# Kernel tuning notes

Hardware: AMD Instinct MI355X
Metric: run time of the kernel (lower is better)

## Reference

```python
import jax, jax.numpy as jnp
import numpy as np

B, S, D, H = 4, 2048, 1024, 16
HD = D // H
SCALE = 1.0 / np.sqrt(HD)
BIG_NEG = -1e9


def setup_inputs() -> dict:
    key = jax.random.key(0)
    ks = jax.random.split(key, 10)
    std = 1.0 / np.sqrt(D)
    return {
        "hidden_states": jax.random.normal(ks[0], (B, S, D), dtype=jnp.float32),
        "attention_mask": jax.random.bernoulli(ks[1], 0.9, (B, S)),
        "Wq": jax.random.normal(ks[2], (D, D), dtype=jnp.float32) * std,
        "bq": jnp.zeros((D,), jnp.float32),
        "Wk": jax.random.normal(ks[3], (D, D), dtype=jnp.float32) * std,
        "bk": jnp.zeros((D,), jnp.float32),
        "Wv": jax.random.normal(ks[4], (D, D), dtype=jnp.float32) * std,
        "bv": jnp.zeros((D,), jnp.float32),
        "Wo": jax.random.normal(ks[5], (D, D), dtype=jnp.float32) * std,
        "bo": jnp.zeros((D,), jnp.float32),
    }


def reference(hidden_states, attention_mask, Wq, bq, Wk, bk, Wv, bv, Wo, bo):
    b, s, d = hidden_states.shape
    maskf = attention_mask.astype(hidden_states.dtype)  # [B,S]
    x = hidden_states * maskf[:, :, None]  # mask inputs (as in torch fallback)

    def proj(W, bias):
        # torch Linear: x @ W.T + b, then split heads -> [B,H,S,HD]
        y = jnp.einsum('bsd,ed->bse', x, W) + bias
        return y.reshape(b, s, H, HD).transpose(0, 2, 1, 3)

    q = proj(Wq, bq)
    k = proj(Wk, bk)
    v = proj(Wv, bv)

    scores = jnp.einsum('bhqd,bhkd->bhqk', q, k) * SCALE  # [B,H,S,S]
    pair = attention_mask[:, None, :, None] & attention_mask[:, None, None, :]
    scores = jnp.where(pair, scores, BIG_NEG)
    # softmax; fully-masked query rows become uniform, then zeroed below
    # (matches torch's -inf softmax -> NaN -> nan_to_num(0.0))
    w = jax.nn.softmax(scores, axis=-1) * maskf[:, None, :, None]
    ctx = jnp.einsum('bhqk,bhkd->bhqd', w, v)  # [B,H,S,HD]
    ctx = ctx.transpose(0, 2, 1, 3).reshape(b, s, d)
    out = jnp.einsum('bsd,ed->bse', ctx, Wo) + bo
    return out * maskf[:, :, None]
```

## Files before the change

kernel.cpp:

```cpp
#include <hip/hip_runtime.h>
#include <math.h>


typedef __attribute__((ext_vector_type(4))) float f32x4;
typedef __attribute__((ext_vector_type(8))) short s16x8;

#define MFMA16(a, b, c) __builtin_amdgcn_mfma_f32_16x16x32_bf16((a), (b), (c), 0, 0, 0)

constexpr int B_ = 4, S_ = 2048, D_ = 1024, H_ = 16, HD_ = 64;
constexpr float SCALE_ = 0.125f;
constexpr float LOG2E_ = 1.4426950408889634f;
constexpr float BIG_NEG_ = -1e9f;
constexpr float DEFER_THR_ = 8.f;

__device__ __forceinline__ ushort f2b(float x) {
    unsigned u = __float_as_uint(x);
    return (ushort)((u + 0x7FFFu + ((u >> 16) & 1u)) >> 16);
}

__device__ __forceinline__ void gload16(const ushort* g, ushort* l) {
    __builtin_amdgcn_global_load_lds(
        (const __attribute__((address_space(1))) void*)g,
        (__attribute__((address_space(3))) void*)l, 16, 0, 0);
}

__global__ __launch_bounds__(256)
void convert_all(const float* __restrict__ hidden, const int* __restrict__ mask,
                 const float* __restrict__ Wq, const float* __restrict__ Wk,
                 const float* __restrict__ Wv, const float* __restrict__ Wo,
                 ushort* __restrict__ Xb, ushort* __restrict__ Wb)
{
    const int NXC = 1048576;
    const int NWC = 131072;
    const int TOT = NXC + 4 * NWC;
    for (int idx = blockIdx.x * 256 + threadIdx.x; idx < TOT; idx += gridDim.x * 256) {
        if (idx < NXC) {
            const size_t e = (size_t)idx * 8;
            const float mf = (float)mask[e >> 10];
            const float4 a = *(const float4*)(hidden + e);
            const float4 b = *(const float4*)(hidden + e + 4);
            s16x8 v;
            v[0] = (short)f2b(a.x * mf); v[1] = (short)f2b(a.y * mf);
            v[2] = (short)f2b(a.z * mf); v[3] = (short)f2b(a.w * mf);
            v[4] = (short)f2b(b.x * mf); v[5] = (short)f2b(b.y * mf);
            v[6] = (short)f2b(b.z * mf); v[7] = (short)f2b(b.w * mf);
            *(s16x8*)(Xb + e) = v;
        } else {
            const int c = idx - NXC;
            const int sel = c >> 17;
            const size_t off = (size_t)(c & (NWC - 1)) * 8;
            const float* src = (sel == 0) ? Wq : (sel == 1) ? Wk : (sel == 2) ? Wv : Wo;
            const float4 a = *(const float4*)(src + off);
            const float4 b = *(const float4*)(src + off + 4);
            s16x8 v;
            v[0] = (short)f2b(a.x); v[1] = (short)f2b(a.y);
            v[2] = (short)f2b(a.z); v[3] = (short)f2b(a.w);
            v[4] = (short)f2b(b.x); v[5] = (short)f2b(b.y);
            v[6] = (short)f2b(b.z); v[7] = (short)f2b(b.w);
            *(s16x8*)(Wb + (size_t)sel * 1048576 + off) = v;
        }
    }
}

__global__ __launch_bounds__(256)
void qkv_gemm(const ushort* __restrict__ Xb, const ushort* __restrict__ Wall,
              const float* __restrict__ bq, const float* __restrict__ bk,
              const float* __restrict__ bv,
              ushort* __restrict__ Qb, ushort* __restrict__ Kb,
              ushort* __restrict__ Vb)
{
    __shared__ ushort As[128 * 64];
    __shared__ ushort Bs[128 * 64];

    const int t = threadIdx.x;
    const int lane = t & 63;
    const int w = t >> 6, wr = w >> 1, wc = w & 1;
    const int lrow = lane & 15, lk = lane >> 4;
    const int m0 = blockIdx.x * 128;
    const int sel = blockIdx.y >> 3;
    const int n0 = (blockIdx.y & 7) * 128;

    const ushort* Wb = Wall + (size_t)sel * 1048576;
    const float* bias = (sel == 0) ? bq : (sel == 1) ? bk : bv;
    ushort* Out = (sel == 0) ? Qb : (sel == 1) ? Kb : Vb;
    const float escale = (sel == 0) ? SCALE_ * LOG2E_ : 1.f;

    f32x4 acc[4][4];
    #pragma unroll
    for (int i = 0; i < 4; ++i)
        #pragma unroll
        for (int j = 0; j < 4; ++j) acc[i][j] = (f32x4)0.f;

    for (int k0 = 0; k0 < D_; k0 += 64) {
        __syncthreads();
        #pragma unroll
        for (int p = 0; p < 4; ++p) {
            const int c = p * 256 + t;
            const int row = c >> 3, slot = c & 7;
            ushort* dst_base_a = As + (size_t)(p * 256 + (t & 192)) * 8;
            ushort* dst_base_b = Bs + (size_t)(p * 256 + (t & 192)) * 8;
            gload16(Xb + (size_t)(m0 + row) * 1024 + k0 + slot * 8, dst_base_a);
            gload16(Wb + (size_t)(n0 + row) * 1024 + k0 + slot * 8, dst_base_b);
        }
        __syncthreads();

        #pragma unroll
        for (int kk = 0; kk < 2; ++kk) {
            s16x8 af[4], bf[4];
            #pragma unroll
            for (int i = 0; i < 4; ++i)
                af[i] = *(const s16x8*)(As + (wr * 64 + i * 16 + lrow) * 64 + kk * 32 + lk * 8);
            #pragma unroll
            for (int j = 0; j < 4; ++j)
                bf[j] = *(const s16x8*)(Bs + (wc * 64 + j * 16 + lrow) * 64 + kk * 32 + lk * 8);
            #pragma unroll
            for (int i = 0; i < 4; ++i)
                #pragma unroll
                for (int j = 0; j < 4; ++j)
                    acc[i][j] = MFMA16(af[i], bf[j], acc[i][j]);
        }
    }

    #pragma unroll
    for (int i = 0; i < 4; ++i) {
        #pragma unroll
        for (int j = 0; j < 4; ++j) {
            const int gn = n0 + wc * 64 + j * 16 + lrow;
            const float bb = bias[gn];
            const int h_ = gn >> 6, hd_ = gn & 63;
            #pragma unroll
            for (int r = 0; r < 4; ++r) {
                const int gm = m0 + wr * 64 + i * 16 + lk * 4 + r;
                const float v = (acc[i][j][r] + bb) * escale;
                const int b_ = gm >> 11, s_ = gm & (S_ - 1);
                Out[(((size_t)(b_ * H_ + h_)) * S_ + s_) * HD_ + hd_] = f2b(v);
            }
        }
    }
}

__global__ __launch_bounds__(256)
void transpose_v(const ushort* __restrict__ V, ushort* __restrict__ VT)
{
    __shared__ ushort L[64][72];
    const int t = threadIdx.x;
    const int s0 = blockIdx.x * 64;
    const size_t base = ((size_t)(blockIdx.z * H_ + blockIdx.y)) * S_ * HD_;
    const int r = t >> 2, cb = (t & 3) * 16;

    *(s16x8*)&L[r][cb]     = *(const s16x8*)(V + base + (size_t)(s0 + r) * 64 + cb);
    *(s16x8*)&L[r][cb + 8] = *(const s16x8*)(V + base + (size_t)(s0 + r) * 64 + cb + 8);
    __syncthreads();

    s16x8 o0, o1;
    #pragma unroll
    for (int k = 0; k < 8; ++k) o0[k] = (short)L[cb + k][r];
    #pragma unroll
    for (int k = 0; k < 8; ++k) o1[k] = (short)L[cb + 8 + k][r];
    *(s16x8*)(VT + base + (size_t)r * S_ + s0 + cb)     = o0;
    *(s16x8*)(VT + base + (size_t)r * S_ + s0 + cb + 8) = o1;
}

__global__ __launch_bounds__(256)
void attn_bf16(const ushort* __restrict__ Q, const ushort* __restrict__ K,
               const ushort* __restrict__ VT, const int* __restrict__ mask,
               ushort* __restrict__ ctx)
{
    __shared__ ushort Ks[64 * 64];
    __shared__ ushort Vs[64 * 64];
    __shared__ ushort Ps[4][16 * 64];

    const int t = threadIdx.x;
    const int lane = t & 63, w = t >> 6;
    const int lrow = lane & 15, lk = lane >> 4;
    const int q0 = blockIdx.x * 64, h = blockIdx.y, b = blockIdx.z;

    const ushort* Qh = Q + ((size_t)(b * H_ + h)) * S_ * HD_;
    const ushort* Kh = K + ((size_t)(b * H_ + h)) * S_ * HD_;
    const ushort* Vh = VT + ((size_t)(b * H_ + h)) * HD_ * S_;
    const int* mrow = mask + b * S_;

    s16x8 qf[2];
    qf[0] = *(const s16x8*)(Qh + (q0 + w * 16 + lrow) * 64 + lk * 8);
    qf[1] = *(const s16x8*)(Qh + (q0 + w * 16 + lrow) * 64 + 32 + lk * 8);

    f32x4 O[4];
    #pragma unroll
    for (int nt = 0; nt < 4; ++nt) O[nt] = (f32x4)0.f;
    float m_run[4] = {-INFINITY, -INFINITY, -INFINITY, -INFINITY};
    float l_run[4] = {0.f, 0.f, 0.f, 0.f};

    const int srow0 = t >> 3,           sslot0 = t & 7;
    const int srow1 = (t + 256) >> 3,   sslot1 = t & 7;
    s16x8 kreg0, kreg1, vreg0, vreg1;
    kreg0 = *(const s16x8*)(Kh + (size_t)srow0 * 64 + sslot0 * 8);
    kreg1 = *(const s16x8*)(Kh + (size_t)srow1 * 64 + sslot1 * 8);
    vreg0 = *(const s16x8*)(Vh + (size_t)srow0 * S_ + sslot0 * 8);
    vreg1 = *(const s16x8*)(Vh + (size_t)srow1 * S_ + sslot1 * 8);

    for (int k0 = 0; k0 < S_; k0 += 64) {
        __syncthreads();
        *(s16x8*)(Ks + srow0 * 64 + ((sslot0 ^ (srow0 & 7)) * 8)) = kreg0;
        *(s16x8*)(Ks + srow1 * 64 + ((sslot1 ^ (srow1 & 7)) * 8)) = kreg1;
        *(s16x8*)(Vs + srow0 * 64 + ((sslot0 ^ (srow0 & 7)) * 8)) = vreg0;
        *(s16x8*)(Vs + srow1 * 64 + ((sslot1 ^ (srow1 & 7)) * 8)) = vreg1;
        __syncthreads();

        if (k0 + 64 < S_) {
            kreg0 = *(const s16x8*)(Kh + (size_t)(k0 + 64 + srow0) * 64 + sslot0 * 8);
            kreg1 = *(const s16x8*)(Kh + (size_t)(k0 + 64 + srow1) * 64 + sslot1 * 8);
            vreg0 = *(const s16x8*)(Vh + (size_t)srow0 * S_ + k0 + 64 + sslot0 * 8);
            vreg1 = *(const s16x8*)(Vh + (size_t)srow1 * S_ + k0 + 64 + sslot1 * 8);
        }

        f32x4 sc[4];
        #pragma unroll
        for (int nt = 0; nt < 4; ++nt) sc[nt] = (f32x4)0.f;
        #pragma unroll
        for (int kk = 0; kk < 2; ++kk)
            #pragma unroll
            for (int nt = 0; nt < 4; ++nt) {
                const int krow = nt * 16 + lrow;
                const s16x8 kf = *(const s16x8*)(Ks + krow * 64 + (((kk * 4 + lk) ^ (krow & 7)) * 8));
                sc[nt] = MFMA16(qf[kk], kf, sc[nt]);
            }

        int km[4];
        #pragma unroll
        for (int nt = 0; nt < 4; ++nt) km[nt] = mrow[k0 + nt * 16 + lrow];

        float s4[4][4], vmax[4];
        #pragma unroll
        for (int r = 0; r < 4; ++r) {
            #pragma unroll
            for (int nt = 0; nt < 4; ++nt) s4[r][nt] = km[nt] ? sc[nt][r] : BIG_NEG_;
            float tm = fmaxf(fmaxf(s4[r][0], s4[r][1]), fmaxf(s4[r][2], s4[r][3]));
            tm = fmaxf(tm, __shfl_xor(tm, 1));
            tm = fmaxf(tm, __shfl_xor(tm, 2));
            tm = fmaxf(tm, __shfl_xor(tm, 4));
            tm = fmaxf(tm, __shfl_xor(tm, 8));
            vmax[r] = tm;
        }

        float g = vmax[0] - m_run[0];
        #pragma unroll
        for (int r = 1; r < 4; ++r) g = fmaxf(g, vmax[r] - m_run[r]);
        if (!__all(g <= DEFER_THR_)) {
            #pragma unroll
            for (int r = 0; r < 4; ++r) {
                const float mn = fmaxf(m_run[r], vmax[r]);
                const float corr = exp2f(m_run[r] - mn);
                m_run[r] = mn;
                l_run[r] *= corr;
                #pragma unroll
                for (int nt = 0; nt < 4; ++nt) O[nt][r] *= corr;
            }
        }

        float pv[4][4];
        #pragma unroll
        for (int r = 0; r < 4; ++r) {
            float rs = 0.f;
            #pragma unroll
            for (int nt = 0; nt < 4; ++nt) {
                pv[r][nt] = exp2f(s4[r][nt] - m_run[r]);
                rs += pv[r][nt];
            }
            rs += __shfl_xor(rs, 1);
            rs += __shfl_xor(rs, 2);
            rs += __shfl_xor(rs, 4);
            rs += __shfl_xor(rs, 8);
            l_run[r] += rs;
        }

        #pragma unroll
        for (int r = 0; r < 4; ++r) {
            const int q = lk * 4 + r;
            #pragma unroll
            for (int nt = 0; nt < 4; ++nt) {
                const int key = nt * 16 + lrow;
                Ps[w][q * 64 + (((key >> 3) ^ (q & 7)) * 8) + (key & 7)] = f2b(pv[r][nt]);
            }
        }
        #pragma unroll
        for (int kk = 0; kk < 2; ++kk) {
            const s16x8 pa = *(const s16x8*)(&Ps[w][lrow * 64 + (((kk * 4 + lk) ^ (lrow & 7)) * 8)]);
            #pragma unroll
            for (int nt = 0; nt < 4; ++nt) {
                const int vrow = nt * 16 + lrow;
                const s16x8 vf = *(const s16x8*)(Vs + vrow * 64 + (((kk * 4 + lk) ^ (vrow & 7)) * 8));
                O[nt] = MFMA16(pa, vf, O[nt]);
            }
        }
    }

    #pragma unroll
    for (int r = 0; r < 4; ++r) {
        const float inv = 1.f / l_run[r];
        const int s = q0 + w * 16 + lk * 4 + r;
        #pragma unroll
        for (int nt = 0; nt < 4; ++nt)
            ctx[((size_t)(b * S_ + s)) * D_ + h * 64 + nt * 16 + lrow] = f2b(O[nt][r] * inv);
    }
}

__global__ __launch_bounds__(256)
void out_gemm(const ushort* __restrict__ Xb, const ushort* __restrict__ Wb,
              const float* __restrict__ bias, const int* __restrict__ mask,
              float* __restrict__ Cf)
{
    __shared__ ushort As[128 * 64];
    __shared__ ushort Bs[128 * 64];

    const int t = threadIdx.x;
    const int lane = t & 63;
    const int w = t >> 6, wr = w >> 1, wc = w & 1;
    const int lrow = lane & 15, lk = lane >> 4;
    const int m0 = blockIdx.x * 128, n0 = blockIdx.y * 128;

    f32x4 acc[4][4];
    #pragma unroll
    for (int i = 0; i < 4; ++i)
        #pragma unroll
        for (int j = 0; j < 4; ++j) acc[i][j] = (f32x4)0.f;

    for (int k0 = 0; k0 < D_; k0 += 64) {
        __syncthreads();
        #pragma unroll
        for (int p = 0; p < 4; ++p) {
            const int c = p * 256 + t;
            const int row = c >> 3, slot = c & 7;
            gload16(Xb + (size_t)(m0 + row) * 1024 + k0 + slot * 8,
                    As + (size_t)(p * 256 + (t & 192)) * 8);
            gload16(Wb + (size_t)(n0 + row) * 1024 + k0 + slot * 8,
                    Bs + (size_t)(p * 256 + (t & 192)) * 8);
        }
        __syncthreads();

        #pragma unroll
        for (int kk = 0; kk < 2; ++kk) {
            s16x8 af[4], bf[4];
            #pragma unroll
            for (int i = 0; i < 4; ++i)
                af[i] = *(const s16x8*)(As + (wr * 64 + i * 16 + lrow) * 64 + kk * 32 + lk * 8);
            #pragma unroll
            for (int j = 0; j < 4; ++j)
                bf[j] = *(const s16x8*)(Bs + (wc * 64 + j * 16 + lrow) * 64 + kk * 32 + lk * 8);
            #pragma unroll
            for (int i = 0; i < 4; ++i)
                #pragma unroll
                for (int j = 0; j < 4; ++j)
                    acc[i][j] = MFMA16(af[i], bf[j], acc[i][j]);
        }
    }

    #pragma unroll
    for (int i = 0; i < 4; ++i) {
        #pragma unroll
        for (int j = 0; j < 4; ++j) {
            const int gn = n0 + wc * 64 + j * 16 + lrow;
            const float bb = bias[gn];
            #pragma unroll
            for (int r = 0; r < 4; ++r) {
                const int gm = m0 + wr * 64 + i * 16 + lk * 4 + r;
                const float v = (acc[i][j][r] + bb) * (float)mask[gm];
                Cf[(size_t)gm * 1024 + gn] = v;
            }
        }
    }
}

extern "C" void kernel_launch(void* const* d_in, const int* in_sizes, int n_in,
                              void* d_out, int out_size, void* d_ws, size_t ws_size,
                              hipStream_t stream) {
    const float* hidden = (const float*)d_in[0];
    const int*   mask   = (const int*)d_in[1];
    const float* Wq = (const float*)d_in[2];
    const float* bq = (const float*)d_in[3];
    const float* Wk = (const float*)d_in[4];
    const float* bk = (const float*)d_in[5];
    const float* Wv = (const float*)d_in[6];
    const float* bv = (const float*)d_in[7];
    const float* Wo = (const float*)d_in[8];
    const float* bo = (const float*)d_in[9];
    float* out = (float*)d_out;

    ushort* ws = (ushort*)d_ws;
    const size_t T = (size_t)B_ * H_ * S_ * HD_;
    ushort* Xb  = ws;
    ushort* Wb  = ws + T;
    ushort* Qb  = ws + T + 4194304;
    ushort* Kb  = Qb + T;
    ushort* Vb  = Kb + T;
    ushort* VTb = Vb + T;
    ushort* Cb  = VTb + T;

    const dim3 bb(256);
    convert_all<<<2048, bb, 0, stream>>>(hidden, mask, Wq, Wk, Wv, Wo, Xb, Wb);
    qkv_gemm<<<dim3(64, 24), bb, 0, stream>>>(Xb, Wb, bq, bk, bv, Qb, Kb, Vb);
    transpose_v<<<dim3(S_ / 64, H_, B_), bb, 0, stream>>>(Vb, VTb);
    attn_bf16<<<dim3(S_ / 64, H_, B_), bb, 0, stream>>>(Qb, Kb, VTb, mask, Cb);
    out_gemm<<<dim3(64, 8), bb, 0, stream>>>(Cb, Wb + 3 * 1048576, bo, mask, out);
}
```

Baseline: 457.9 us.

## Transpose QK^T MFMA so each lane owns one query row in attention

```diff
diff --git a/kernel.cpp b/kernel.cpp
--- a/kernel.cpp
+++ b/kernel.cpp
@@ -97,10 +97,10 @@
         for (int p = 0; p < 4; ++p) {
             const int c = p * 256 + t;
             const int row = c >> 3, slot = c & 7;
-            ushort* dst_base_a = As + (size_t)(p * 256 + (t & 192)) * 8;
-            ushort* dst_base_b = Bs + (size_t)(p * 256 + (t & 192)) * 8;
-            gload16(Xb + (size_t)(m0 + row) * 1024 + k0 + slot * 8, dst_base_a);
-            gload16(Wb + (size_t)(n0 + row) * 1024 + k0 + slot * 8, dst_base_b);
+            gload16(Xb + (size_t)(m0 + row) * 1024 + k0 + slot * 8,
+                    As + (size_t)(p * 256 + (t & 192)) * 8);
+            gload16(Wb + (size_t)(n0 + row) * 1024 + k0 + slot * 8,
+                    Bs + (size_t)(p * 256 + (t & 192)) * 8);
         }
         __syncthreads();
 
@@ -166,9 +166,9 @@
                const ushort* __restrict__ VT, const int* __restrict__ mask,
                ushort* __restrict__ ctx)
 {
-    __shared__ ushort Ks[64 * 64];
-    __shared__ ushort Vs[64 * 64];
-    __shared__ ushort Ps[4][16 * 64];
+    __shared__ __align__(16) ushort Ks[64 * 64];
+    __shared__ __align__(16) ushort Vs[64 * 64];
+    __shared__ __align__(16) ushort Ps[4][16 * 64];
 
     const int t = threadIdx.x;
     const int lane = t & 63, w = t >> 6;
@@ -187,31 +187,22 @@
     f32x4 O[4];
     #pragma unroll
     for (int nt = 0; nt < 4; ++nt) O[nt] = (f32x4)0.f;
-    float m_run[4] = {-INFINITY, -INFINITY, -INFINITY, -INFINITY};
-    float l_run[4] = {0.f, 0.f, 0.f, 0.f};
-
-    const int srow0 = t >> 3,           sslot0 = t & 7;
-    const int srow1 = (t + 256) >> 3,   sslot1 = t & 7;
-    s16x8 kreg0, kreg1, vreg0, vreg1;
-    kreg0 = *(const s16x8*)(Kh + (size_t)srow0 * 64 + sslot0 * 8);
-    kreg1 = *(const s16x8*)(Kh + (size_t)srow1 * 64 + sslot1 * 8);
-    vreg0 = *(const s16x8*)(Vh + (size_t)srow0 * S_ + sslot0 * 8);
-    vreg1 = *(const s16x8*)(Vh + (size_t)srow1 * S_ + sslot1 * 8);
+    float m_run = -INFINITY;
+    float l_run = 0.f;
+
+    const int srow = t >> 3, sslot = t & 7;
 
     for (int k0 = 0; k0 < S_; k0 += 64) {
         __syncthreads();
-        *(s16x8*)(Ks + srow0 * 64 + ((sslot0 ^ (srow0 & 7)) * 8)) = kreg0;
-        *(s16x8*)(Ks + srow1 * 64 + ((sslot1 ^ (srow1 & 7)) * 8)) = kreg1;
-        *(s16x8*)(Vs + srow0 * 64 + ((sslot0 ^ (srow0 & 7)) * 8)) = vreg0;
-        *(s16x8*)(Vs + srow1 * 64 + ((sslot1 ^ (srow1 & 7)) * 8)) = vreg1;
-        __syncthreads();
-
-        if (k0 + 64 < S_) {
-            kreg0 = *(const s16x8*)(Kh + (size_t)(k0 + 64 + srow0) * 64 + sslot0 * 8);
-            kreg1 = *(const s16x8*)(Kh + (size_t)(k0 + 64 + srow1) * 64 + sslot1 * 8);
-            vreg0 = *(const s16x8*)(Vh + (size_t)srow0 * S_ + k0 + 64 + sslot0 * 8);
-            vreg1 = *(const s16x8*)(Vh + (size_t)srow1 * S_ + k0 + 64 + sslot1 * 8);
-        }
+        #pragma unroll
+        for (int p = 0; p < 2; ++p) {
+            const int row = srow + p * 32;
+            const s16x8 kv = *(const s16x8*)(Kh + (size_t)(k0 + row) * 64 + sslot * 8);
+            *(s16x8*)(Ks + row * 64 + ((sslot ^ (row & 7)) * 8)) = kv;
+            const s16x8 vv = *(const s16x8*)(Vh + (size_t)row * S_ + k0 + sslot * 8);
+            *(s16x8*)(Vs + row * 64 + ((sslot ^ (row & 7)) * 8)) = vv;
+        }
+        __syncthreads();
 
         f32x4 sc[4];
         #pragma unroll
@@ -222,66 +213,60 @@
             for (int nt = 0; nt < 4; ++nt) {
                 const int krow = nt * 16 + lrow;
                 const s16x8 kf = *(const s16x8*)(Ks + krow * 64 + (((kk * 4 + lk) ^ (krow & 7)) * 8));
-                sc[nt] = MFMA16(qf[kk], kf, sc[nt]);
+                sc[nt] = MFMA16(kf, qf[kk], sc[nt]);
             }
 
-        int km[4];
-        #pragma unroll
-        for (int nt = 0; nt < 4; ++nt) km[nt] = mrow[k0 + nt * 16 + lrow];
-
-        float s4[4][4], vmax[4];
-        #pragma unroll
-        for (int r = 0; r < 4; ++r) {
-            #pragma unroll
-            for (int nt = 0; nt < 4; ++nt) s4[r][nt] = km[nt] ? sc[nt][r] : BIG_NEG_;
-            float tm = fmaxf(fmaxf(s4[r][0], s4[r][1]), fmaxf(s4[r][2], s4[r][3]));
-            tm = fmaxf(tm, __shfl_xor(tm, 1));
-            tm = fmaxf(tm, __shfl_xor(tm, 2));
-            tm = fmaxf(tm, __shfl_xor(tm, 4));
-            tm = fmaxf(tm, __shfl_xor(tm, 8));
-            vmax[r] = tm;
-        }
-
-        float g = vmax[0] - m_run[0];
-        #pragma unroll
-        for (int r = 1; r < 4; ++r) g = fmaxf(g, vmax[r] - m_run[r]);
-        if (!__all(g <= DEFER_THR_)) {
-            #pragma unroll
-            for (int r = 0; r < 4; ++r) {
-                const float mn = fmaxf(m_run[r], vmax[r]);
-                const float corr = exp2f(m_run[r] - mn);
-                m_run[r] = mn;
-                l_run[r] *= corr;
+        float s4[4][4];
+        #pragma unroll
+        for (int nt = 0; nt < 4; ++nt) {
+            const int4 km = *(const int4*)(mrow + k0 + nt * 16 + lk * 4);
+            s4[nt][0] = km.x ? sc[nt][0] : BIG_NEG_;
+            s4[nt][1] = km.y ? sc[nt][1] : BIG_NEG_;
+            s4[nt][2] = km.z ? sc[nt][2] : BIG_NEG_;
+            s4[nt][3] = km.w ? sc[nt][3] : BIG_NEG_;
+        }
+
+        float tm = s4[0][0];
+        #pragma unroll
+        for (int nt = 0; nt < 4; ++nt)
+            #pragma unroll
+            for (int r = 0; r < 4; ++r) tm = fmaxf(tm, s4[nt][r]);
+        tm = fmaxf(tm, __shfl_xor(tm, 16));
+        tm = fmaxf(tm, __shfl_xor(tm, 32));
+
+        if (!__all(tm - m_run <= DEFER_THR_)) {
+            const float mn = fmaxf(m_run, tm);
+            const float corr = exp2f(m_run - mn);
+            m_run = mn;
+            l_run *= corr;
+            float cq[4];
+            #pragma unroll
+            for (int r = 0; r < 4; ++r) cq[r] = __shfl(corr, lk * 4 + r);
+            #pragma unroll
+            for (int nt = 0; nt < 4; ++nt)
                 #pragma unroll
-                for (int nt = 0; nt < 4; ++nt) O[nt][r] *= corr;
-            }
-        }
-
-        float pv[4][4];
-        #pragma unroll
-        for (int r = 0; r < 4; ++r) {
-            float rs = 0.f;
-            #pragma unroll
-            for (int nt = 0; nt < 4; ++nt) {
-                pv[r][nt] = exp2f(s4[r][nt] - m_run[r]);
-                rs += pv[r][nt];
-            }
-            rs += __shfl_xor(rs, 1);
-            rs += __shfl_xor(rs, 2);
-            rs += __shfl_xor(rs, 4);
-            rs += __shfl_xor(rs, 8);
-            l_run[r] += rs;
-        }
-
-        #pragma unroll
-        for (int r = 0; r < 4; ++r) {
-            const int q = lk * 4 + r;
-            #pragma unroll
-            for (int nt = 0; nt < 4; ++nt) {
-                const int key = nt * 16 + lrow;
-                Ps[w][q * 64 + (((key >> 3) ^ (q & 7)) * 8) + (key & 7)] = f2b(pv[r][nt]);
-            }
-        }
+                for (int r = 0; r < 4; ++r) O[nt][r] *= cq[r];
+        }
+
+        float p[4][4];
+        float rs = 0.f;
+        #pragma unroll
+        for (int nt = 0; nt < 4; ++nt)
+            #pragma unroll
+            for (int r = 0; r < 4; ++r) { p[nt][r] = exp2f(s4[nt][r] - m_run); rs += p[nt][r]; }
+        rs += __shfl_xor(rs, 16);
+        rs += __shfl_xor(rs, 32);
+        l_run += rs;
+
+        #pragma unroll
+        for (int nt = 0; nt < 4; ++nt) {
+            uint2 w2;
+            w2.x = ((uint)f2b(p[nt][1]) << 16) | f2b(p[nt][0]);
+            w2.y = ((uint)f2b(p[nt][3]) << 16) | f2b(p[nt][2]);
+            const int slot = (nt * 2 + (lk >> 1)) ^ (lrow & 7);
+            *(uint2*)(&Ps[w][lrow * 64 + slot * 8 + 4 * (lk & 1)]) = w2;
+        }
+
         #pragma unroll
         for (int kk = 0; kk < 2; ++kk) {
             const s16x8 pa = *(const s16x8*)(&Ps[w][lrow * 64 + (((kk * 4 + lk) ^ (lrow & 7)) * 8)]);
@@ -294,13 +279,16 @@
         }
     }
 
+    const float inv = 1.f / l_run;
+    float invq[4];
+    #pragma unroll
+    for (int r = 0; r < 4; ++r) invq[r] = __shfl(inv, lk * 4 + r);
     #pragma unroll
     for (int r = 0; r < 4; ++r) {
-        const float inv = 1.f / l_run[r];
         const int s = q0 + w * 16 + lk * 4 + r;
         #pragma unroll
         for (int nt = 0; nt < 4; ++nt)
-            ctx[((size_t)(b * S_ + s)) * D_ + h * 64 + nt * 16 + lrow] = f2b(O[nt][r] * inv);
+            ctx[((size_t)(b * S_ + s)) * D_ + h * 64 + nt * 16 + lrow] = f2b(O[nt][r] * invq[r]);
     }
 }
 
```

Result: faster. 386.7 us (-15.6%).
